# Optimization experiments

Hardware: AMD Instinct MI355X
Metric: run time of the kernel (lower is better)

Reference implementation:

```python
import jax, jax.numpy as jnp
import numpy as np

HEAD = 8
DIM_HEAD = 64
EPS = 1e-5  # torch GroupNorm default


def group_norm(x, w, b, groups, eps=EPS):
    # x: [B, C, H, W]; normalize per (group, spatial)
    B, C, H, W = x.shape
    xg = x.reshape(B, groups, C // groups, H, W)
    mu = xg.mean(axis=(2, 3, 4), keepdims=True)
    var = xg.var(axis=(2, 3, 4), keepdims=True)
    xn = ((xg - mu) / jnp.sqrt(var + eps)).reshape(B, C, H, W)
    return xn * w[None, :, None, None] + b[None, :, None, None]


def setup_inputs() -> dict:
    key = jax.random.key(0)
    ks = jax.random.split(key, 4)
    dim = 256
    hidden = HEAD * DIM_HEAD  # 512
    x = jax.random.normal(ks[0], (16, dim, 64, 64), dtype=jnp.float32)
    qkv_w = jax.random.normal(ks[1], (hidden * 3, dim), dtype=jnp.float32) * 0.02
    out_w = jax.random.normal(ks[2], (dim, hidden), dtype=jnp.float32) * 0.02
    out_b = jnp.zeros((dim,), dtype=jnp.float32)
    gn1_w = jnp.ones((dim,), dtype=jnp.float32)
    gn1_b = jnp.zeros((dim,), dtype=jnp.float32)
    gn2_w = jnp.ones((dim,), dtype=jnp.float32)
    gn2_b = jnp.zeros((dim,), dtype=jnp.float32)
    return {"x": x, "gn1_w": gn1_w, "gn1_b": gn1_b, "qkv_w": qkv_w,
            "out_w": out_w, "out_b": out_b, "gn2_w": gn2_w, "gn2_b": gn2_b}


def reference(x, gn1_w, gn1_b, qkv_w, out_w, out_b, gn2_w, gn2_b):
    B, C, I, J = x.shape
    groups = C // 8
    scale = DIM_HEAD ** -0.5
    n = I * J

    xn = group_norm(x, gn1_w, gn1_b, groups)
    # 1x1 conv == channel matmul: [B,3*hidden,I,J]
    qkv = jnp.einsum('bchw,oc->bohw', xn, qkv_w)
    q, k, v = jnp.split(qkv, 3, axis=1)

    def to_heads(t):  # [B, h*f, I, J] -> [B, h, f, n]
        return t.reshape(B, HEAD, DIM_HEAD, n)

    q = jax.nn.softmax(to_heads(q), axis=-2) * scale  # softmax over feature dim
    k = jax.nn.softmax(to_heads(k), axis=-1)          # softmax over spatial dim
    v = to_heads(v)

    context = jnp.einsum('bhfm,bhem->bhfe', k, v)     # [B,h,f,e]
    attn = jnp.einsum('bhfe,bhfn->bhen', context, q)  # [B,h,e,n]
    out = attn.reshape(B, HEAD * DIM_HEAD, I, J)

    out = jnp.einsum('bchw,oc->bohw', out, out_w) + out_b[None, :, None, None]
    return group_norm(out, gn2_w, gn2_b, groups)
```

## Files before the change

kernel.cpp:

```cpp
#include <hip/hip_runtime.h>
#include <math.h>

#define NB   16
#define NC   256
#define NP   4096
#define NHD  8
#define FD   64
#define HID  512
#define OC3  1536
#define NG   32
#define CPG  8
#define GEPS 1e-5f

typedef __attribute__((ext_vector_type(8))) short bf16x8;
typedef __attribute__((ext_vector_type(4))) float f32x4;

#define MFMA_BF16(a, b, c) __builtin_amdgcn_mfma_f32_16x16x32_bf16(a, b, c, 0, 0, 0)

__device__ __forceinline__ uint bf16_rne(float v) {
    uint u = __float_as_uint(v);
    return (u + 0x7FFFu + ((u >> 16) & 1u)) >> 16;
}
__device__ __forceinline__ void split2(float v, uint& h, uint& l) {
    h = bf16_rne(v);
    l = bf16_rne(v - __uint_as_float(h << 16));
}
__device__ __forceinline__ void gload16(const void* g, void* l) {
    __builtin_amdgcn_global_load_lds(
        (const __attribute__((address_space(1))) void*)g,
        (__attribute__((address_space(3))) void*)l, 16, 0, 0);
}

__global__ __launch_bounds__(256) void gn_stats_kernel(const float* __restrict__ x,
                                                       float* __restrict__ mu,
                                                       float* __restrict__ rstd) {
    int bg = blockIdx.x;
    const float4* b4 = (const float4*)(x + (size_t)bg * CPG * NP);
    int t = threadIdx.x;
    float s = 0.f, sq = 0.f;
    #pragma unroll
    for (int i = 0; i < 32; ++i) {
        float4 v = b4[t + i * 256];
        s  += v.x + v.y + v.z + v.w;
        sq += v.x*v.x + v.y*v.y + v.z*v.z + v.w*v.w;
    }
    for (int off = 32; off; off >>= 1) { s += __shfl_down(s, off); sq += __shfl_down(sq, off); }
    __shared__ float ss[4], ssq[4];
    int wid = t >> 6, lane = t & 63;
    if (lane == 0) { ss[wid] = s; ssq[wid] = sq; }
    __syncthreads();
    if (t == 0) {
        float S  = ss[0] + ss[1] + ss[2] + ss[3];
        float SQ = ssq[0] + ssq[1] + ssq[2] + ssq[3];
        const float inv = 1.f / (float)(CPG * NP);
        float m = S * inv;
        float var = SQ * inv - m * m;
        mu[bg] = m;
        rstd[bg] = rsqrtf(var + GEPS);
    }
}

__global__ void gn1_coefs_kernel(const float* __restrict__ mu, const float* __restrict__ rstd,
                                 const float* __restrict__ w, const float* __restrict__ bias,
                                 float* __restrict__ ac, float* __restrict__ dc) {
    int i = blockIdx.x * 256 + threadIdx.x;
    if (i >= NB * NC) return;
    int b = i / NC, c = i % NC;
    int g = c / CPG;
    float m = mu[b * NG + g], r = rstd[b * NG + g];
    float a = r * w[c];
    ac[i] = a;
    dc[i] = bias[c] - m * a;
}

__global__ void wsplit_kernel(const float* __restrict__ w, ushort* __restrict__ wh,
                              ushort* __restrict__ wl) {
    int i = blockIdx.x * 256 + threadIdx.x;
    float4 v = ((const float4*)w)[i];
    uint h, l;
    ushort4 hv, lv;
    split2(v.x, h, l); hv.x = (ushort)h; lv.x = (ushort)l;
    split2(v.y, h, l); hv.y = (ushort)h; lv.y = (ushort)l;
    split2(v.z, h, l); hv.z = (ushort)h; lv.z = (ushort)l;
    split2(v.w, h, l); hv.w = (ushort)h; lv.w = (ushort)l;
    ((ushort4*)wh)[i] = hv;
    ((ushort4*)wl)[i] = lv;
}

__global__ __launch_bounds__(256) void xsplit_kernel(const float* __restrict__ x,
                                                     const float* __restrict__ ac,
                                                     const float* __restrict__ dc,
                                                     ushort* __restrict__ xTh,
                                                     ushort* __restrict__ xTl, int b0) {
    int z = blockIdx.z, bglob = b0 + z;
    int p0 = blockIdx.x * 64, c0 = blockIdx.y * 64;
    const float* xb = x + (size_t)bglob * NC * NP;
    __shared__ float T[64][68];
    int t = threadIdx.x;
    #pragma unroll
    for (int j = 0; j < 4; ++j) {
        int idx = t + j * 256;
        int r = idx >> 4, c4 = idx & 15;
        float4 v = *(const float4*)(xb + (size_t)(c0 + r) * NP + p0 + c4 * 4);
        float a = ac[bglob * NC + c0 + r], d = dc[bglob * NC + c0 + r];
        v.x = fmaf(v.x, a, d); v.y = fmaf(v.y, a, d);
        v.z = fmaf(v.z, a, d); v.w = fmaf(v.w, a, d);
        *(float4*)&T[r][c4 * 4] = v;
    }
    __syncthreads();
    int p = t & 63, q4 = t >> 6;
    size_t ob = ((size_t)z * NP + p0 + p) * NC + c0 + q4 * 16;
    #pragma unroll
    for (int blk = 0; blk < 2; ++blk) {
        uint4 uh, ul;
        uint* ph = (uint*)&uh; uint* pl = (uint*)&ul;
        #pragma unroll
        for (int i = 0; i < 4; ++i) {
            int c = q4 * 16 + blk * 8 + i * 2;
            uint h0, l0, h1, l1;
            split2(T[c][p], h0, l0);
            split2(T[c + 1][p], h1, l1);
            ph[i] = h0 | (h1 << 16);
            pl[i] = l0 | (l1 << 16);
        }
        *(uint4*)(xTh + ob + blk * 8) = uh;
        *(uint4*)(xTl + ob + blk * 8) = ul;
    }
}

__global__ __launch_bounds__(256) void gemm_q_kernel(
        const ushort* __restrict__ Ah, const ushort* __restrict__ Al,
        const ushort* __restrict__ Bhg, const ushort* __restrict__ Blg,
        ushort* __restrict__ qsTh, ushort* __restrict__ qsTl) {
    __shared__ __align__(16) char smem[33280];
    const int z = blockIdx.z;
    const ushort* Bh = Bhg + (size_t)NP * NC * z;
    const ushort* Bl = Blg + (size_t)NP * NC * z;

    const int t = threadIdx.x;
    const int w = t >> 6, l = t & 63;
    const int wr = w >> 1, wc = w & 1;
    const int m0 = blockIdx.y * 128, n0 = blockIdx.x * 128;
    const int l15 = l & 15, kb = l >> 4;

    f32x4 acc[4][4];
    #pragma unroll
    for (int i = 0; i < 4; ++i)
        #pragma unroll
        for (int j = 0; j < 4; ++j)
            acc[i][j] = (f32x4){0.f, 0.f, 0.f, 0.f};

    for (int k0 = 0; k0 < NC; k0 += 32) {
        #pragma unroll
        for (int j = 0; j < 2; ++j) {
            int idx = t + j * 256;
            int m = idx & 127, s = idx >> 7;
            size_t goA = (size_t)(m0 + m) * NC + k0 + s * 8;
            size_t goB = (size_t)(n0 + m) * NC + k0 + s * 8;
            int lo = idx * 16;
            gload16(Ah + goA, smem + lo);
            gload16(Al + goA, smem + 8192 + lo);
            gload16(Bh + goB, smem + 16384 + lo);
            gload16(Bl + goB, smem + 24576 + lo);
        }
        __syncthreads();
        bf16x8 ah[4], al[4];
        #pragma unroll
        for (int fi = 0; fi < 4; ++fi) {
            int off = (kb * 128 + wr * 64 + fi * 16 + l15) * 16;
            ah[fi] = *(const bf16x8*)(smem + off);
            al[fi] = *(const bf16x8*)(smem + 8192 + off);
        }
        #pragma unroll
        for (int fj = 0; fj < 4; ++fj) {
            int off = (kb * 128 + wc * 64 + fj * 16 + l15) * 16;
            bf16x8 bh = *(const bf16x8*)(smem + 16384 + off);
            bf16x8 bl = *(const bf16x8*)(smem + 24576 + off);
            #pragma unroll
            for (int fi = 0; fi < 4; ++fi) {
                acc[fi][fj] = MFMA_BF16(ah[fi], bh, acc[fi][fj]);
                acc[fi][fj] = MFMA_BF16(al[fi], bh, acc[fi][fj]);
                acc[fi][fj] = MFMA_BF16(ah[fi], bl, acc[fi][fj]);
            }
        }
        __syncthreads();
    }

    uint* Tq = (uint*)smem;
    #pragma unroll
    for (int half = 0; half < 2; ++half) {
        if (wc == half) {
            #pragma unroll
            for (int fj = 0; fj < 4; ++fj) {
                float ex[16];
                float cs = 0.f;
                #pragma unroll
                for (int fi = 0; fi < 4; ++fi)
                    #pragma unroll
                    for (int r = 0; r < 4; ++r) {
                        float e = __expf(acc[fi][fj][r]);
                        ex[fi * 4 + r] = e;
                        cs += e;
                    }
                cs += __shfl_xor(cs, 16);
                cs += __shfl_xor(cs, 32);
                float inv = 0.125f / cs;
                int p_loc = fj * 16 + l15;
                #pragma unroll
                for (int fi = 0; fi < 4; ++fi)
                    #pragma unroll
                    for (int r = 0; r < 4; ++r) {
                        uint hb, lb;
                        split2(ex[fi * 4 + r] * inv, hb, lb);
                        Tq[p_loc * 130 + wr * 64 + fi * 16 + kb * 4 + r] = (hb << 16) | lb;
                    }
            }
        }
        __syncthreads();
        int p = t >> 2, seg = t & 3;
        size_t ob = ((size_t)z * NP + n0 + half * 64 + p) * HID + m0 + seg * 32;
        #pragma unroll
        for (int c = 0; c < 4; ++c) {
            uint4 H, L;
            uint* hp = (uint*)&H; uint* lp = (uint*)&L;
            #pragma unroll
            for (int i = 0; i < 4; ++i) {
                uint u0 = Tq[p * 130 + seg * 32 + c * 8 + 2 * i];
                uint u1 = Tq[p * 130 + seg * 32 + c * 8 + 2 * i + 1];
                hp[i] = (u0 >> 16) | (u1 & 0xffff0000u);
                lp[i] = (u0 & 0xffffu) | (u1 << 16);
            }
            *(uint4*)(qsTh + ob + c * 8) = H;
            *(uint4*)(qsTl + ob + c * 8) = L;
        }
        __syncthreads();
    }
}

__global__ __launch_bounds__(256) void kv_ctx_kernel(
        const ushort* __restrict__ Wh, const ushort* __restrict__ Wl,
        const ushort* __restrict__ Bhg, const ushort* __restrict__ Blg,
        float* __restrict__ ctxp, float* __restrict__ kspart) {
    __shared__ __align__(16) char smem[69632];
    const int z = blockIdx.z;
    const int h = blockIdx.y;
    const int tile = blockIdx.x;
    const int n0 = tile * 128;
    const ushort* Bh = Bhg + (size_t)NP * NC * z;
    const ushort* Bl = Blg + (size_t)NP * NC * z;

    const int t = threadIdx.x;
    const int w = t >> 6, l = t & 63;
    const int wr = w >> 1, wc = w & 1;
    const int l15 = l & 15, kb = l >> 4;

    ushort* ekh = (ushort*)smem;
    ushort* ekl = ekh + 64 * 136;
    ushort* vh_ = ekl + 64 * 136;
    ushort* vl_ = vh_ + 64 * 136;

    f32x4 acc[4][4];
    #pragma unroll
    for (int i = 0; i < 4; ++i)
        #pragma unroll
        for (int j = 0; j < 4; ++j)
            acc[i][j] = (f32x4){0.f, 0.f, 0.f, 0.f};

    for (int k0 = 0; k0 < NC; k0 += 32) {
        #pragma unroll
        for (int j = 0; j < 2; ++j) {
            int idx = t + j * 256;
            int m = idx & 127, s = idx >> 7;
            int grow = 512 + h * 64 + (m & 63) + ((m >> 6) << 9);
            size_t goA = (size_t)grow * NC + k0 + s * 8;
            size_t goB = (size_t)(n0 + m) * NC + k0 + s * 8;
            int lo = idx * 16;
            gload16(Wh + goA, smem + lo);
            gload16(Wl + goA, smem + 8192 + lo);
            gload16(Bh + goB, smem + 16384 + lo);
            gload16(Bl + goB, smem + 24576 + lo);
        }
        __syncthreads();
        bf16x8 ah[4], al[4];
        #pragma unroll
        for (int fi = 0; fi < 4; ++fi) {
            int off = (kb * 128 + wr * 64 + fi * 16 + l15) * 16;
            ah[fi] = *(const bf16x8*)(smem + off);
            al[fi] = *(const bf16x8*)(smem + 8192 + off);
        }
        #pragma unroll
        for (int fj = 0; fj < 4; ++fj) {
            int off = (kb * 128 + wc * 64 + fj * 16 + l15) * 16;
            bf16x8 bh = *(const bf16x8*)(smem + 16384 + off);
            bf16x8 bl = *(const bf16x8*)(smem + 24576 + off);
            #pragma unroll
            for (int fi = 0; fi < 4; ++fi) {
                acc[fi][fj] = MFMA_BF16(ah[fi], bh, acc[fi][fj]);
                acc[fi][fj] = MFMA_BF16(al[fi], bh, acc[fi][fj]);
                acc[fi][fj] = MFMA_BF16(ah[fi], bl, acc[fi][fj]);
            }
        }
        __syncthreads();
    }

    #pragma unroll
    for (int fi = 0; fi < 4; ++fi) {
        #pragma unroll
        for (int r = 0; r < 4; ++r) {
            int row = fi * 16 + kb * 4 + r;
            float rs = 0.f;
            #pragma unroll
            for (int fj = 0; fj < 4; ++fj) {
                float v = acc[fi][fj][r];
                float e = (wr == 0) ? __expf(v) : v;
                rs += e;
                uint hb, lb;
                split2(e, hb, lb);
                int P = wc * 64 + fj * 16 + l15;
                if (wr == 0) { ekh[row * 136 + P] = (ushort)hb; ekl[row * 136 + P] = (ushort)lb; }
                else         { vh_[row * 136 + P] = (ushort)hb; vl_[row * 136 + P] = (ushort)lb; }
            }
            if (wr == 0) {
                rs += __shfl_xor(rs, 1); rs += __shfl_xor(rs, 2);
                rs += __shfl_xor(rs, 4); rs += __shfl_xor(rs, 8);
                if (l15 == 0)
                    kspart[((size_t)z * HID + h * 64 + row) * 64 + tile * 2 + wc] = rs;
            }
        }
    }
    __syncthreads();

    f32x4 c2[2][2];
    #pragma unroll
    for (int i = 0; i < 2; ++i)
        #pragma unroll
        for (int j = 0; j < 2; ++j)
            c2[i][j] = (f32x4){0.f, 0.f, 0.f, 0.f};
    #pragma unroll
    for (int ks = 0; ks < 4; ++ks) {
        bf16x8 a_h[2], a_l[2], b_h[2], b_l[2];
        #pragma unroll
        for (int i = 0; i < 2; ++i) {
            int offa = (wr * 32 + i * 16 + l15) * 136 + ks * 32 + kb * 8;
            a_h[i] = *(const bf16x8*)(ekh + offa);
            a_l[i] = *(const bf16x8*)(ekl + offa);
            int offb = (wc * 32 + i * 16 + l15) * 136 + ks * 32 + kb * 8;
            b_h[i] = *(const bf16x8*)(vh_ + offb);
            b_l[i] = *(const bf16x8*)(vl_ + offb);
        }
        #pragma unroll
        for (int i = 0; i < 2; ++i)
            #pragma unroll
            for (int j = 0; j < 2; ++j) {
                c2[i][j] = MFMA_BF16(a_h[i], b_h[j], c2[i][j]);
                c2[i][j] = MFMA_BF16(a_l[i], b_h[j], c2[i][j]);
                c2[i][j] = MFMA_BF16(a_h[i], b_l[j], c2[i][j]);
            }
    }
    float* outp = ctxp + (((size_t)z * NHD + h) * 32 + tile) * 4096;
    #pragma unroll
    for (int i = 0; i < 2; ++i)
        #pragma unroll
        for (int j = 0; j < 2; ++j)
            #pragma unroll
            for (int r = 0; r < 4; ++r)
                outp[(size_t)(wr * 32 + i * 16 + kb * 4 + r) * 64 + wc * 32 + j * 16 + l15] = c2[i][j][r];
}

__global__ void ksum_reduce_kernel(const float* __restrict__ kspart,
                                   float* __restrict__ ksum, int n) {
    int i = blockIdx.x * 256 + threadIdx.x;
    if (i >= n) return;
    float s = 0.f;
    #pragma unroll
    for (int j = 0; j < 64; ++j) s += kspart[(size_t)i * 64 + j];
    ksum[i] = s;
}

__global__ void ctx_reduce_kernel(const float* __restrict__ ctxp, float* __restrict__ ctx,
                                  int n4) {
    int i = blockIdx.x * 256 + threadIdx.x;
    if (i >= n4) return;
    int zh = i >> 10, i4 = i & 1023;
    const float4* p = (const float4*)ctxp + (size_t)zh * 32 * 1024;
    float4 r = {0.f, 0.f, 0.f, 0.f};
    #pragma unroll
    for (int s = 0; s < 32; ++s) {
        float4 a = p[(size_t)s * 1024 + i4];
        r.x += a.x; r.y += a.y; r.z += a.z; r.w += a.w;
    }
    ((float4*)ctx)[(size_t)zh * 1024 + i4] = r;
}

__global__ __launch_bounds__(256) void fold_kernel(const float* __restrict__ out_w,
                                                   const float* __restrict__ ctx,
                                                   const float* __restrict__ ksum,
                                                   ushort* __restrict__ w2h,
                                                   ushort* __restrict__ w2l) {
    int h = blockIdx.x, z = blockIdx.y;
    __shared__ float Cs[FD][FD];
    int t = threadIdx.x;
    const float* cbase = ctx + ((size_t)z * NHD + h) * FD * FD;
    #pragma unroll
    for (int j = 0; j < 16; ++j) ((float*)Cs)[t + j * 256] = cbase[t + j * 256];
    __syncthreads();
    float wr[64];
    const float* wrow = out_w + (size_t)t * HID + h * FD;
    #pragma unroll
    for (int e = 0; e < 64; ++e) wr[e] = wrow[e];
    size_t ob = ((size_t)z * NC + t) * HID + h * FD;
    for (int f = 0; f < 64; ++f) {
        float sacc = 0.f;
        #pragma unroll
        for (int e = 0; e < 64; ++e) sacc = fmaf(wr[e], Cs[f][e], sacc);
        float v = sacc / ksum[(size_t)z * HID + h * FD + f];
        uint hb, lb;
        split2(v, hb, lb);
        w2h[ob + f] = (ushort)hb;
        w2l[ob + f] = (ushort)lb;
    }
}

__global__ __launch_bounds__(256) void gemm_out_kernel(
        const ushort* __restrict__ Ahg, const ushort* __restrict__ Alg,
        const ushort* __restrict__ Bhg, const ushort* __restrict__ Blg,
        const float* __restrict__ bias, float* __restrict__ outg,
        float2* __restrict__ gn2part, int b0) {
    __shared__ __align__(16) char smem[32768];
    const int z = blockIdx.z, bglob = b0 + z;
    const ushort* Ah = Ahg + (size_t)NC * HID * z;
    const ushort* Al = Alg + (size_t)NC * HID * z;
    const ushort* Bh = Bhg + (size_t)NP * HID * z;
    const ushort* Bl = Blg + (size_t)NP * HID * z;
    float* C = outg + (size_t)bglob * NC * NP;

    const int t = threadIdx.x;
    const int w = t >> 6, l = t & 63;
    const int wr = w >> 1, wc = w & 1;
    const int m0 = blockIdx.y * 128, n0 = blockIdx.x * 128;
    const int l15 = l & 15, kb = l >> 4;

    f32x4 acc[4][4];
    #pragma unroll
    for (int i = 0; i < 4; ++i)
        #pragma unroll
        for (int j = 0; j < 4; ++j)
            acc[i][j] = (f32x4){0.f, 0.f, 0.f, 0.f};

    for (int k0 = 0; k0 < HID; k0 += 32) {
        #pragma unroll
        for (int j = 0; j < 2; ++j) {
            int idx = t + j * 256;
            int m = idx & 127, s = idx >> 7;
            size_t goA = (size_t)(m0 + m) * HID + k0 + s * 8;
            size_t goB = (size_t)(n0 + m) * HID + k0 + s * 8;
            int lo = idx * 16;
            gload16(Ah + goA, smem + lo);
            gload16(Al + goA, smem + 8192 + lo);
            gload16(Bh + goB, smem + 16384 + lo);
            gload16(Bl + goB, smem + 24576 + lo);
        }
        __syncthreads();
        bf16x8 ah[4], al[4];
        #pragma unroll
        for (int fi = 0; fi < 4; ++fi) {
            int off = (kb * 128 + wr * 64 + fi * 16 + l15) * 16;
            ah[fi] = *(const bf16x8*)(smem + off);
            al[fi] = *(const bf16x8*)(smem + 8192 + off);
        }
        #pragma unroll
        for (int fj = 0; fj < 4; ++fj) {
            int off = (kb * 128 + wc * 64 + fj * 16 + l15) * 16;
            bf16x8 bh = *(const bf16x8*)(smem + 16384 + off);
            bf16x8 bl = *(const bf16x8*)(smem + 24576 + off);
            #pragma unroll
            for (int fi = 0; fi < 4; ++fi) {
                acc[fi][fj] = MFMA_BF16(ah[fi], bh, acc[fi][fj]);
                acc[fi][fj] = MFMA_BF16(al[fi], bh, acc[fi][fj]);
                acc[fi][fj] = MFMA_BF16(ah[fi], bl, acc[fi][fj]);
            }
        }
        __syncthreads();
    }

    float gs[4] = {0.f, 0.f, 0.f, 0.f}, gq[4] = {0.f, 0.f, 0.f, 0.f};
    #pragma unroll
    for (int fi = 0; fi < 4; ++fi) {
        int mbase = m0 + wr * 64 + fi * 16 + kb * 4;
        #pragma unroll
        for (int fj = 0; fj < 4; ++fj) {
            int n = n0 + wc * 64 + fj * 16 + l15;
            #pragma unroll
            for (int r = 0; r < 4; ++r) {
                float v = acc[fi][fj][r] + bias[mbase + r];
                C[(size_t)(mbase + r) * NP + n] = v;
                gs[fi] += v;
                gq[fi] += v * v;
            }
        }
    }
    #pragma unroll
    for (int fi = 0; fi < 4; ++fi) {
        #pragma unroll
        for (int d = 1; d <= 16; d <<= 1) {
            gs[fi] += __shfl_xor(gs[fi], d);
            gq[fi] += __shfl_xor(gq[fi], d);
        }
    }
    if (l15 == 0 && (kb & 1) == 0) {
        #pragma unroll
        for (int fi = 0; fi < 4; ++fi) {
            int g = ((m0 + wr * 64) >> 3) + fi * 2 + (kb >> 1);
            float2 pv; pv.x = gs[fi]; pv.y = gq[fi];
            gn2part[(((size_t)bglob * NG + g) << 6) + blockIdx.x * 2 + wc] = pv;
        }
    }
}

__global__ void gn2_reduce_kernel(const float2* __restrict__ gn2part,
                                  float* __restrict__ mu, float* __restrict__ rstd) {
    int i = blockIdx.x * 256 + threadIdx.x;
    if (i >= NB * NG) return;
    float s = 0.f, q = 0.f;
    #pragma unroll
    for (int j = 0; j < 64; ++j) {
        float2 p = gn2part[((size_t)i << 6) + j];
        s += p.x; q += p.y;
    }
    const float inv = 1.f / (float)(CPG * NP);
    float m = s * inv;
    float var = q * inv - m * m;
    mu[i] = m;
    rstd[i] = rsqrtf(var + GEPS);
}

__global__ void gn2_apply_kernel(float* __restrict__ out, const float* __restrict__ mu,
                                 const float* __restrict__ rstd, const float* __restrict__ w,
                                 const float* __restrict__ bias) {
    int i = blockIdx.x * 256 + threadIdx.x;
    float4* p = (float4*)out;
    float4 v = p[i];
    size_t e0 = (size_t)i * 4;
    int cidx = (int)((e0 / NP) % NC);
    int bg   = (int)(e0 / ((size_t)CPG * NP));
    float m = mu[bg], r = rstd[bg];
    float a = r * w[cidx];
    float d = bias[cidx] - m * a;
    v.x = fmaf(v.x, a, d); v.y = fmaf(v.y, a, d);
    v.z = fmaf(v.z, a, d); v.w = fmaf(v.w, a, d);
    p[i] = v;
}

extern "C" void kernel_launch(void* const* d_in, const int* in_sizes, int n_in,
                              void* d_out, int out_size, void* d_ws, size_t ws_size,
                              hipStream_t stream) {
    const float* x     = (const float*)d_in[0];
    const float* gn1_w = (const float*)d_in[1];
    const float* gn1_b = (const float*)d_in[2];
    const float* qkv_w = (const float*)d_in[3];
    const float* out_w = (const float*)d_in[4];
    const float* out_b = (const float*)d_in[5];
    const float* gn2_w = (const float*)d_in[6];
    const float* gn2_b = (const float*)d_in[7];
    float* out = (float*)d_out;

    auto need = [](int cb) -> size_t {
        size_t tot = 0;
        auto al = [&](size_t b) { tot = (tot + b + 255) & ~(size_t)255; };
        al((size_t)cb * NP * NC * 2);  al((size_t)cb * NP * NC * 2);
        al((size_t)cb * NP * HID * 2); al((size_t)cb * NP * HID * 2);
        al((size_t)cb * NHD * 32 * FD * FD * 4);
        al((size_t)cb * NHD * FD * FD * 4);
        al((size_t)cb * HID * 64 * 4);
        al((size_t)cb * HID * 4);
        al((size_t)cb * NC * HID * 2); al((size_t)cb * NC * HID * 2);
        al((size_t)OC3 * NC * 2); al((size_t)OC3 * NC * 2);
        al((size_t)2 * NB * NC * 4);
        al((size_t)4 * NB * NG * 4);
        al((size_t)NB * NG * 64 * 8);
        return tot;
    };
    int CB = 1;
    {
        const int cands[5] = {16, 8, 4, 2, 1};
        for (int i = 0; i < 5; ++i) if (need(cands[i]) <= ws_size) { CB = cands[i]; break; }
    }

    char* base = (char*)d_ws;
    size_t off = 0;
    auto carve = [&](size_t b) -> char* {
        char* p = base + off;
        off = (off + b + 255) & ~(size_t)255;
        return p;
    };
    ushort* xTh  = (ushort*)carve((size_t)CB * NP * NC * 2);
    ushort* xTl  = (ushort*)carve((size_t)CB * NP * NC * 2);
    ushort* qsTh = (ushort*)carve((size_t)CB * NP * HID * 2);
    ushort* qsTl = (ushort*)carve((size_t)CB * NP * HID * 2);
    float*  ctxp = (float*) carve((size_t)CB * NHD * 32 * FD * FD * 4);
    float*  ctx  = (float*) carve((size_t)CB * NHD * FD * FD * 4);
    float*  kspart = (float*)carve((size_t)CB * HID * 64 * 4);
    float*  ksum = (float*) carve((size_t)CB * HID * 4);
    ushort* w2h  = (ushort*)carve((size_t)CB * NC * HID * 2);
    ushort* w2l  = (ushort*)carve((size_t)CB * NC * HID * 2);
    ushort* Wqh  = (ushort*)carve((size_t)OC3 * NC * 2);
    ushort* Wql  = (ushort*)carve((size_t)OC3 * NC * 2);
    float*  ac   = (float*) carve((size_t)2 * NB * NC * 4);
    float*  dc   = ac + (size_t)NB * NC;
    float*  mu1  = (float*) carve((size_t)4 * NB * NG * 4);
    float*  rstd1 = mu1 + NB * NG;
    float*  mu2   = rstd1 + NB * NG;
    float*  rstd2 = mu2 + NB * NG;
    float2* gn2part = (float2*)carve((size_t)NB * NG * 64 * 8);

    gn_stats_kernel<<<NB * NG, 256, 0, stream>>>(x, mu1, rstd1);
    gn1_coefs_kernel<<<16, 256, 0, stream>>>(mu1, rstd1, gn1_w, gn1_b, ac, dc);
    wsplit_kernel<<<OC3 * NC / 1024, 256, 0, stream>>>(qkv_w, Wqh, Wql);

    for (int b0 = 0; b0 < NB; b0 += CB) {
        xsplit_kernel<<<dim3(NP / 64, NC / 64, CB), 256, 0, stream>>>(x, ac, dc, xTh, xTl, b0);
        gemm_q_kernel<<<dim3(NP / 128, 4, CB), 256, 0, stream>>>(Wqh, Wql, xTh, xTl, qsTh, qsTl);
        kv_ctx_kernel<<<dim3(NP / 128, NHD, CB), 256, 0, stream>>>(Wqh, Wql, xTh, xTl, ctxp, kspart);
        ksum_reduce_kernel<<<(CB * HID + 255) / 256, 256, 0, stream>>>(kspart, ksum, CB * HID);
        ctx_reduce_kernel<<<CB * 32, 256, 0, stream>>>(ctxp, ctx, CB * NHD * 1024);
        fold_kernel<<<dim3(NHD, CB), 256, 0, stream>>>(out_w, ctx, ksum, w2h, w2l);
        gemm_out_kernel<<<dim3(NP / 128, 2, CB), 256, 0, stream>>>(
            w2h, w2l, qsTh, qsTl, out_b, out, gn2part, b0);
    }

    gn2_reduce_kernel<<<2, 256, 0, stream>>>(gn2part, mu2, rstd2);
    gn2_apply_kernel<<<16384, 256, 0, stream>>>(out, mu2, rstd2, gn2_w, gn2_b);
}
```

Baseline: 583.6 us.

## Fold GroupNorm1 affine into per-batch QKV weights and fuse stats into split pass

The separate GroupNorm1 stats pass over x is removed. Group statistics are now accumulated inside the transpose/split kernel, which stores raw x as bf16 hi/lo. The per-channel scale is folded into per-batch copies of the QKV weight, and the shift becomes a per-output bias added before the softmax in the q and kv GEMM epilogues. The kv_ctx K-loop also moves to a K-step of 64 with larger shared memory, halving barrier count. This trades one full read of x for per-batch weight splitting and bias kernels, plus more workspace and occupancy pressure in kv_ctx.

Result: slower. 640.8 us (+9.8%).

```diff
diff --git a/kernel.cpp b/kernel.cpp
--- a/kernel.cpp
+++ b/kernel.cpp
@@ -31,109 +31,135 @@
         (__attribute__((address_space(3))) void*)l, 16, 0, 0);
 }
 
-__global__ __launch_bounds__(256) void gn_stats_kernel(const float* __restrict__ x,
-                                                       float* __restrict__ mu,
-                                                       float* __restrict__ rstd) {
-    int bg = blockIdx.x;
-    const float4* b4 = (const float4*)(x + (size_t)bg * CPG * NP);
+__global__ __launch_bounds__(256) void xstats_split_kernel(const float* __restrict__ x,
+                                                           ushort* __restrict__ xTh,
+                                                           ushort* __restrict__ xTl,
+                                                           float2* __restrict__ gn1part, int b0) {
+    int z = blockIdx.z, bglob = b0 + z;
+    int p0 = blockIdx.x * 64, c0 = blockIdx.y * 64;
+    const float* xb = x + (size_t)bglob * NC * NP;
+    __shared__ float T[64][72];
+    __shared__ float rs[64], rq[64];
     int t = threadIdx.x;
-    float s = 0.f, sq = 0.f;
-    #pragma unroll
-    for (int i = 0; i < 32; ++i) {
-        float4 v = b4[t + i * 256];
-        s  += v.x + v.y + v.z + v.w;
-        sq += v.x*v.x + v.y*v.y + v.z*v.z + v.w*v.w;
-    }
-    for (int off = 32; off; off >>= 1) { s += __shfl_down(s, off); sq += __shfl_down(sq, off); }
-    __shared__ float ss[4], ssq[4];
-    int wid = t >> 6, lane = t & 63;
-    if (lane == 0) { ss[wid] = s; ssq[wid] = sq; }
+    #pragma unroll
+    for (int j = 0; j < 4; ++j) {
+        int idx = t + j * 256;
+        int r = idx >> 4, c4 = idx & 15;
+        float4 v = *(const float4*)(xb + (size_t)(c0 + r) * NP + p0 + c4 * 4);
+        *(float4*)&T[r][c4 * 4] = v;
+    }
     __syncthreads();
-    if (t == 0) {
-        float S  = ss[0] + ss[1] + ss[2] + ss[3];
-        float SQ = ssq[0] + ssq[1] + ssq[2] + ssq[3];
-        const float inv = 1.f / (float)(CPG * NP);
-        float m = S * inv;
-        float var = SQ * inv - m * m;
-        mu[bg] = m;
-        rstd[bg] = rsqrtf(var + GEPS);
-    }
+    {
+        int row = t >> 2, quad = t & 3;
+        float s = 0.f, q = 0.f;
+        #pragma unroll
+        for (int j = 0; j < 16; ++j) { float v = T[row][quad * 16 + j]; s += v; q += v * v; }
+        s += __shfl_xor(s, 1); q += __shfl_xor(q, 1);
+        s += __shfl_xor(s, 2); q += __shfl_xor(q, 2);
+        if (quad == 0) { rs[row] = s; rq[row] = q; }
+    }
+    __syncthreads();
+    if (t < 8) {
+        float S = 0.f, Q = 0.f;
+        #pragma unroll
+        for (int k = 0; k < 8; ++k) { S += rs[t * 8 + k]; Q += rq[t * 8 + k]; }
+        gn1part[((size_t)z * NG + blockIdx.y * 8 + t) * 64 + blockIdx.x] = make_float2(S, Q);
+    }
+    int p = t >> 2, cseg = t & 3;
+    size_t ob = ((size_t)z * NP + p0 + p) * NC + c0 + cseg * 16;
+    #pragma unroll
+    for (int half = 0; half < 2; ++half) {
+        uint4 uh, ul;
+        uint* ph = (uint*)&uh; uint* pl = (uint*)&ul;
+        #pragma unroll
+        for (int i = 0; i < 4; ++i) {
+            int c = cseg * 16 + half * 8 + i * 2;
+            uint h0, l0, h1, l1;
+            split2(T[c][p], h0, l0);
+            split2(T[c + 1][p], h1, l1);
+            ph[i] = h0 | (h1 << 16);
+            pl[i] = l0 | (l1 << 16);
+        }
+        *(uint4*)(xTh + ob + half * 8) = uh;
+        *(uint4*)(xTl + ob + half * 8) = ul;
+    }
+}
+
+__global__ void gn1_reduce_kernel(const float2* __restrict__ gn1part,
+                                  float* __restrict__ mu, float* __restrict__ rstd,
+                                  int b0, int n) {
+    int i = blockIdx.x * 256 + threadIdx.x;
+    if (i >= n) return;
+    float S = 0.f, Q = 0.f;
+    #pragma unroll
+    for (int j = 0; j < 64; ++j) {
+        float2 p = gn1part[(size_t)i * 64 + j];
+        S += p.x; Q += p.y;
+    }
+    const float inv = 1.f / (float)(CPG * NP);
+    float m = S * inv;
+    float var = Q * inv - m * m;
+    mu[b0 * NG + i] = m;
+    rstd[b0 * NG + i] = rsqrtf(var + GEPS);
 }
 
 __global__ void gn1_coefs_kernel(const float* __restrict__ mu, const float* __restrict__ rstd,
                                  const float* __restrict__ w, const float* __restrict__ bias,
-                                 float* __restrict__ ac, float* __restrict__ dc) {
+                                 float* __restrict__ ac, float* __restrict__ dc,
+                                 int b0, int n) {
     int i = blockIdx.x * 256 + threadIdx.x;
-    if (i >= NB * NC) return;
-    int b = i / NC, c = i % NC;
+    if (i >= n) return;
+    int bglob = b0 + i / NC, c = i % NC;
     int g = c / CPG;
-    float m = mu[b * NG + g], r = rstd[b * NG + g];
+    float m = mu[bglob * NG + g], r = rstd[bglob * NG + g];
     float a = r * w[c];
-    ac[i] = a;
-    dc[i] = bias[c] - m * a;
-}
-
-__global__ void wsplit_kernel(const float* __restrict__ w, ushort* __restrict__ wh,
-                              ushort* __restrict__ wl) {
-    int i = blockIdx.x * 256 + threadIdx.x;
-    float4 v = ((const float4*)w)[i];
+    ac[(size_t)bglob * NC + c] = a;
+    dc[(size_t)bglob * NC + c] = bias[c] - m * a;
+}
+
+__global__ void wsplit_z_kernel(const float* __restrict__ w, const float* __restrict__ ac,
+                                ushort* __restrict__ Wqzh, ushort* __restrict__ Wqzl, int b0) {
+    int z = blockIdx.y, bglob = b0 + z;
+    int idx = blockIdx.x * 256 + threadIdx.x;
+    float4 v = ((const float4*)w)[idx];
+    int c4 = (idx & 63) * 4;
+    float4 a = *(const float4*)(ac + (size_t)bglob * NC + c4);
+    v.x *= a.x; v.y *= a.y; v.z *= a.z; v.w *= a.w;
     uint h, l;
     ushort4 hv, lv;
     split2(v.x, h, l); hv.x = (ushort)h; lv.x = (ushort)l;
     split2(v.y, h, l); hv.y = (ushort)h; lv.y = (ushort)l;
     split2(v.z, h, l); hv.z = (ushort)h; lv.z = (ushort)l;
     split2(v.w, h, l); hv.w = (ushort)h; lv.w = (ushort)l;
-    ((ushort4*)wh)[i] = hv;
-    ((ushort4*)wl)[i] = lv;
-}
-
-__global__ __launch_bounds__(256) void xsplit_kernel(const float* __restrict__ x,
-                                                     const float* __restrict__ ac,
-                                                     const float* __restrict__ dc,
-                                                     ushort* __restrict__ xTh,
-                                                     ushort* __restrict__ xTl, int b0) {
-    int z = blockIdx.z, bglob = b0 + z;
-    int p0 = blockIdx.x * 64, c0 = blockIdx.y * 64;
-    const float* xb = x + (size_t)bglob * NC * NP;
-    __shared__ float T[64][68];
-    int t = threadIdx.x;
-    #pragma unroll
-    for (int j = 0; j < 4; ++j) {
-        int idx = t + j * 256;
-        int r = idx >> 4, c4 = idx & 15;
-        float4 v = *(const float4*)(xb + (size_t)(c0 + r) * NP + p0 + c4 * 4);
-        float a = ac[bglob * NC + c0 + r], d = dc[bglob * NC + c0 + r];
-        v.x = fmaf(v.x, a, d); v.y = fmaf(v.y, a, d);
-        v.z = fmaf(v.z, a, d); v.w = fmaf(v.w, a, d);
-        *(float4*)&T[r][c4 * 4] = v;
-    }
-    __syncthreads();
-    int p = t & 63, q4 = t >> 6;
-    size_t ob = ((size_t)z * NP + p0 + p) * NC + c0 + q4 * 16;
-    #pragma unroll
-    for (int blk = 0; blk < 2; ++blk) {
-        uint4 uh, ul;
-        uint* ph = (uint*)&uh; uint* pl = (uint*)&ul;
-        #pragma unroll
-        for (int i = 0; i < 4; ++i) {
-            int c = q4 * 16 + blk * 8 + i * 2;
-            uint h0, l0, h1, l1;
-            split2(T[c][p], h0, l0);
-            split2(T[c + 1][p], h1, l1);
-            ph[i] = h0 | (h1 << 16);
-            pl[i] = l0 | (l1 << 16);
-        }
-        *(uint4*)(xTh + ob + blk * 8) = uh;
-        *(uint4*)(xTl + ob + blk * 8) = ul;
-    }
+    ((ushort4*)(Wqzh + (size_t)z * OC3 * NC))[idx] = hv;
+    ((ushort4*)(Wqzl + (size_t)z * OC3 * NC))[idx] = lv;
+}
+
+__global__ void bias2_kernel(const float* __restrict__ w, const float* __restrict__ dc,
+                             float* __restrict__ bias2, int b0) {
+    int i = blockIdx.x * 256 + threadIdx.x;
+    int z = i / OC3, m = i % OC3;
+    int bglob = b0 + z;
+    const float4* w4 = (const float4*)(w + (size_t)m * NC);
+    const float4* d4 = (const float4*)(dc + (size_t)bglob * NC);
+    float s = 0.f;
+    #pragma unroll
+    for (int j = 0; j < 64; ++j) {
+        float4 a = w4[j], b = d4[j];
+        s += a.x * b.x + a.y * b.y + a.z * b.z + a.w * b.w;
+    }
+    bias2[(size_t)z * OC3 + m] = s;
 }
 
 __global__ __launch_bounds__(256) void gemm_q_kernel(
-        const ushort* __restrict__ Ah, const ushort* __restrict__ Al,
+        const ushort* __restrict__ Ahg, const ushort* __restrict__ Alg,
         const ushort* __restrict__ Bhg, const ushort* __restrict__ Blg,
+        const float* __restrict__ bias2,
         ushort* __restrict__ qsTh, ushort* __restrict__ qsTl) {
     __shared__ __align__(16) char smem[33280];
     const int z = blockIdx.z;
+    const ushort* Ah = Ahg + (size_t)OC3 * NC * z;
+    const ushort* Al = Alg + (size_t)OC3 * NC * z;
     const ushort* Bh = Bhg + (size_t)NP * NC * z;
     const ushort* Bl = Blg + (size_t)NP * NC * z;
 
@@ -186,6 +212,16 @@
         __syncthreads();
     }
 
+    float b2v[4][4];
+    {
+        const float* b2z = bias2 + (size_t)z * OC3 + m0 + wr * 64 + kb * 4;
+        #pragma unroll
+        for (int fi = 0; fi < 4; ++fi)
+            #pragma unroll
+            for (int r = 0; r < 4; ++r)
+                b2v[fi][r] = b2z[fi * 16 + r];
+    }
+
     uint* Tq = (uint*)smem;
     #pragma unroll
     for (int half = 0; half < 2; ++half) {
@@ -198,7 +234,7 @@
                 for (int fi = 0; fi < 4; ++fi)
                     #pragma unroll
                     for (int r = 0; r < 4; ++r) {
-                        float e = __expf(acc[fi][fj][r]);
+                        float e = __expf(acc[fi][fj][r] + b2v[fi][r]);
                         ex[fi * 4 + r] = e;
                         cs += e;
                     }
@@ -238,14 +274,17 @@
 }
 
 __global__ __launch_bounds__(256) void kv_ctx_kernel(
-        const ushort* __restrict__ Wh, const ushort* __restrict__ Wl,
+        const ushort* __restrict__ Whg, const ushort* __restrict__ Wlg,
         const ushort* __restrict__ Bhg, const ushort* __restrict__ Blg,
+        const float* __restrict__ bias2,
         float* __restrict__ ctxp, float* __restrict__ kspart) {
     __shared__ __align__(16) char smem[69632];
     const int z = blockIdx.z;
     const int h = blockIdx.y;
     const int tile = blockIdx.x;
     const int n0 = tile * 128;
+    const ushort* Wh = Whg + (size_t)OC3 * NC * z;
+    const ushort* Wl = Wlg + (size_t)OC3 * NC * z;
     const ushort* Bh = Bhg + (size_t)NP * NC * z;
     const ushort* Bl = Blg + (size_t)NP * NC * z;
 
@@ -266,9 +305,9 @@
         for (int j = 0; j < 4; ++j)
             acc[i][j] = (f32x4){0.f, 0.f, 0.f, 0.f};
 
-    for (int k0 = 0; k0 < NC; k0 += 32) {
-        #pragma unroll
-        for (int j = 0; j < 2; ++j) {
+    for (int k0 = 0; k0 < NC; k0 += 64) {
+        #pragma unroll
+        for (int j = 0; j < 4; ++j) {
             int idx = t + j * 256;
             int m = idx & 127, s = idx >> 7;
             int grow = 512 + h * 64 + (m & 63) + ((m >> 6) << 9);
@@ -276,31 +315,44 @@
             size_t goB = (size_t)(n0 + m) * NC + k0 + s * 8;
             int lo = idx * 16;
             gload16(Wh + goA, smem + lo);
-            gload16(Wl + goA, smem + 8192 + lo);
-            gload16(Bh + goB, smem + 16384 + lo);
-            gload16(Bl + goB, smem + 24576 + lo);
-        }
-        __syncthreads();
-        bf16x8 ah[4], al[4];
-        #pragma unroll
-        for (int fi = 0; fi < 4; ++fi) {
-            int off = (kb * 128 + wr * 64 + fi * 16 + l15) * 16;
-            ah[fi] = *(const bf16x8*)(smem + off);
-            al[fi] = *(const bf16x8*)(smem + 8192 + off);
-        }
-        #pragma unroll
-        for (int fj = 0; fj < 4; ++fj) {
-            int off = (kb * 128 + wc * 64 + fj * 16 + l15) * 16;
-            bf16x8 bh = *(const bf16x8*)(smem + 16384 + off);
-            bf16x8 bl = *(const bf16x8*)(smem + 24576 + off);
+            gload16(Wl + goA, smem + 16384 + lo);
+            gload16(Bh + goB, smem + 32768 + lo);
+            gload16(Bl + goB, smem + 49152 + lo);
+        }
+        __syncthreads();
+        #pragma unroll
+        for (int half = 0; half < 2; ++half) {
+            bf16x8 ah[4], al[4];
             #pragma unroll
             for (int fi = 0; fi < 4; ++fi) {
-                acc[fi][fj] = MFMA_BF16(ah[fi], bh, acc[fi][fj]);
-                acc[fi][fj] = MFMA_BF16(al[fi], bh, acc[fi][fj]);
-                acc[fi][fj] = MFMA_BF16(ah[fi], bl, acc[fi][fj]);
-            }
-        }
-        __syncthreads();
+                int off = ((half * 4 + kb) * 128 + wr * 64 + fi * 16 + l15) * 16;
+                ah[fi] = *(const bf16x8*)(smem + off);
+                al[fi] = *(const bf16x8*)(smem + 16384 + off);
+            }
+            #pragma unroll
+            for (int fj = 0; fj < 4; ++fj) {
+                int off = ((half * 4 + kb) * 128 + wc * 64 + fj * 16 + l15) * 16;
+                bf16x8 bh = *(const bf16x8*)(smem + 32768 + off);
+                bf16x8 bl = *(const bf16x8*)(smem + 49152 + off);
+                #pragma unroll
+                for (int fi = 0; fi < 4; ++fi) {
+                    acc[fi][fj] = MFMA_BF16(ah[fi], bh, acc[fi][fj]);
+                    acc[fi][fj] = MFMA_BF16(al[fi], bh, acc[fi][fj]);
+                    acc[fi][fj] = MFMA_BF16(ah[fi], bl, acc[fi][fj]);
+                }
+            }
+        }
+        __syncthreads();
+    }
+
+    float b2v[4][4];
+    {
+        const float* b2z = bias2 + (size_t)z * OC3 + 512 + wr * 512 + h * 64 + kb * 4;
+        #pragma unroll
+        for (int fi = 0; fi < 4; ++fi)
+            #pragma unroll
+            for (int r = 0; r < 4; ++r)
+                b2v[fi][r] = b2z[fi * 16 + r];
     }
 
     #pragma unroll
@@ -311,7 +363,7 @@
             float rs = 0.f;
             #pragma unroll
             for (int fj = 0; fj < 4; ++fj) {
-                float v = acc[fi][fj][r];
+                float v = acc[fi][fj][r] + b2v[fi][r];
                 float e = (wr == 0) ? __expf(v) : v;
                 rs += e;
                 uint hb, lb;
@@ -574,7 +626,9 @@
         al((size_t)cb * HID * 64 * 4);
         al((size_t)cb * HID * 4);
         al((size_t)cb * NC * HID * 2); al((size_t)cb * NC * HID * 2);
-        al((size_t)OC3 * NC * 2); al((size_t)OC3 * NC * 2);
+        al((size_t)cb * OC3 * NC * 2); al((size_t)cb * OC3 * NC * 2);
+        al((size_t)cb * OC3 * 4);
+        al((size_t)cb * NG * 64 * 8);
         al((size_t)2 * NB * NC * 4);
         al((size_t)4 * NB * NG * 4);
         al((size_t)NB * NG * 64 * 8);
@@ -603,8 +657,10 @@
     float*  ksum = (float*) carve((size_t)CB * HID * 4);
     ushort* w2h  = (ushort*)carve((size_t)CB * NC * HID * 2);
     ushort* w2l  = (ushort*)carve((size_t)CB * NC * HID * 2);
-    ushort* Wqh  = (ushort*)carve((size_t)OC3 * NC * 2);
-    ushort* Wql  = (ushort*)carve((size_t)OC3 * NC * 2);
+    ushort* Wqzh = (ushort*)carve((size_t)CB * OC3 * NC * 2);
+    ushort* Wqzl = (ushort*)carve((size_t)CB * OC3 * NC * 2);
+    float*  bias2 = (float*)carve((size_t)CB * OC3 * 4);
+    float2* gn1part = (float2*)carve((size_t)CB * NG * 64 * 8);
     float*  ac   = (float*) carve((size_t)2 * NB * NC * 4);
     float*  dc   = ac + (size_t)NB * NC;
     float*  mu1  = (float*) carve((size_t)4 * NB * NG * 4);
@@ -613,14 +669,19 @@
     float*  rstd2 = mu2 + NB * NG;
     float2* gn2part = (float2*)carve((size_t)NB * NG * 64 * 8);
 
-    gn_stats_kernel<<<NB * NG, 256, 0, stream>>>(x, mu1, rstd1);
-    gn1_coefs_kernel<<<16, 256, 0, stream>>>(mu1, rstd1, gn1_w, gn1_b, ac, dc);
-    wsplit_kernel<<<OC3 * NC / 1024, 256, 0, stream>>>(qkv_w, Wqh, Wql);
-
     for (int b0 = 0; b0 < NB; b0 += CB) {
-        xsplit_kernel<<<dim3(NP / 64, NC / 64, CB), 256, 0, stream>>>(x, ac, dc, xTh, xTl, b0);
-        gemm_q_kernel<<<dim3(NP / 128, 4, CB), 256, 0, stream>>>(Wqh, Wql, xTh, xTl, qsTh, qsTl);
-        kv_ctx_kernel<<<dim3(NP / 128, NHD, CB), 256, 0, stream>>>(Wqh, Wql, xTh, xTl, ctxp, kspart);
+        xstats_split_kernel<<<dim3(NP / 64, NC / 64, CB), 256, 0, stream>>>(
+            x, xTh, xTl, gn1part, b0);
+        gn1_reduce_kernel<<<(CB * NG + 255) / 256, 256, 0, stream>>>(
+            gn1part, mu1, rstd1, b0, CB * NG);
+        gn1_coefs_kernel<<<CB, 256, 0, stream>>>(
+            mu1, rstd1, gn1_w, gn1_b, ac, dc, b0, CB * NC);
+        wsplit_z_kernel<<<dim3(384, CB), 256, 0, stream>>>(qkv_w, ac, Wqzh, Wqzl, b0);
+        bias2_kernel<<<6 * CB, 256, 0, stream>>>(qkv_w, dc, bias2, b0);
+        gemm_q_kernel<<<dim3(NP / 128, 4, CB), 256, 0, stream>>>(
+            Wqzh, Wqzl, xTh, xTl, bias2, qsTh, qsTl);
+        kv_ctx_kernel<<<dim3(NP / 128, NHD, CB), 256, 0, stream>>>(
+            Wqzh, Wqzl, xTh, xTl, bias2, ctxp, kspart);
         ksum_reduce_kernel<<<(CB * HID + 255) / 256, 256, 0, stream>>>(kspart, ksum, CB * HID);
         ctx_reduce_kernel<<<CB * 32, 256, 0, stream>>>(ctxp, ctx, CB * NHD * 1024);
         fold_kernel<<<dim3(NHD, CB), 256, 0, stream>>>(out_w, ctx, ksum, w2h, w2l);
```

## Double kv_ctx block to 512 threads and remap xsplit transpose writes

Applied to the files above, without the earlier changes.

kv_ctx_kernel now runs 8 waves per block instead of 4, each handling a 64x32 slice of the accumulator tile. This halves per-thread accumulator registers and lets more waves hide latency. The k-sum partials grow to 128 per row and the reduction is adjusted to match. xsplit_kernel pads its shared tile to 72 columns and remaps threads so that consecutive threads write adjacent channel segments of the same pixel, which should give more contiguous global stores. The risk is extra block-wide synchronisation and changed shared-memory bank access patterns.

Measured after the change: 564.9 us. -3.2%, faster.

```diff
diff --git a/kernel.cpp b/kernel.cpp
--- a/kernel.cpp
+++ b/kernel.cpp
@@ -95,7 +95,7 @@
     int z = blockIdx.z, bglob = b0 + z;
     int p0 = blockIdx.x * 64, c0 = blockIdx.y * 64;
     const float* xb = x + (size_t)bglob * NC * NP;
-    __shared__ float T[64][68];
+    __shared__ float T[64][72];
     int t = threadIdx.x;
     #pragma unroll
     for (int j = 0; j < 4; ++j) {
@@ -108,23 +108,23 @@
         *(float4*)&T[r][c4 * 4] = v;
     }
     __syncthreads();
-    int p = t & 63, q4 = t >> 6;
-    size_t ob = ((size_t)z * NP + p0 + p) * NC + c0 + q4 * 16;
-    #pragma unroll
-    for (int blk = 0; blk < 2; ++blk) {
+    int p = t >> 2, cseg = t & 3;
+    size_t ob = ((size_t)z * NP + p0 + p) * NC + c0 + cseg * 16;
+    #pragma unroll
+    for (int half = 0; half < 2; ++half) {
         uint4 uh, ul;
         uint* ph = (uint*)&uh; uint* pl = (uint*)&ul;
         #pragma unroll
         for (int i = 0; i < 4; ++i) {
-            int c = q4 * 16 + blk * 8 + i * 2;
+            int c = cseg * 16 + half * 8 + i * 2;
             uint h0, l0, h1, l1;
             split2(T[c][p], h0, l0);
             split2(T[c + 1][p], h1, l1);
             ph[i] = h0 | (h1 << 16);
             pl[i] = l0 | (l1 << 16);
         }
-        *(uint4*)(xTh + ob + blk * 8) = uh;
-        *(uint4*)(xTl + ob + blk * 8) = ul;
+        *(uint4*)(xTh + ob + half * 8) = uh;
+        *(uint4*)(xTl + ob + half * 8) = ul;
     }
 }
 
@@ -237,7 +237,7 @@
     }
 }
 
-__global__ __launch_bounds__(256) void kv_ctx_kernel(
+__global__ __launch_bounds__(512, 4) void kv_ctx_kernel(
         const ushort* __restrict__ Wh, const ushort* __restrict__ Wl,
         const ushort* __restrict__ Bhg, const ushort* __restrict__ Blg,
         float* __restrict__ ctxp, float* __restrict__ kspart) {
@@ -251,7 +251,7 @@
 
     const int t = threadIdx.x;
     const int w = t >> 6, l = t & 63;
-    const int wr = w >> 1, wc = w & 1;
+    const int wr = w >> 2, wc = w & 3;
     const int l15 = l & 15, kb = l >> 4;
 
     ushort* ekh = (ushort*)smem;
@@ -259,17 +259,16 @@
     ushort* vh_ = ekl + 64 * 136;
     ushort* vl_ = vh_ + 64 * 136;
 
-    f32x4 acc[4][4];
+    f32x4 acc[4][2];
     #pragma unroll
     for (int i = 0; i < 4; ++i)
         #pragma unroll
-        for (int j = 0; j < 4; ++j)
+        for (int j = 0; j < 2; ++j)
             acc[i][j] = (f32x4){0.f, 0.f, 0.f, 0.f};
 
     for (int k0 = 0; k0 < NC; k0 += 32) {
-        #pragma unroll
-        for (int j = 0; j < 2; ++j) {
-            int idx = t + j * 256;
+        {
+            int idx = t;
             int m = idx & 127, s = idx >> 7;
             int grow = 512 + h * 64 + (m & 63) + ((m >> 6) << 9);
             size_t goA = (size_t)grow * NC + k0 + s * 8;
@@ -289,8 +288,8 @@
             al[fi] = *(const bf16x8*)(smem + 8192 + off);
         }
         #pragma unroll
-        for (int fj = 0; fj < 4; ++fj) {
-            int off = (kb * 128 + wc * 64 + fj * 16 + l15) * 16;
+        for (int fj = 0; fj < 2; ++fj) {
+            int off = (kb * 128 + wc * 32 + fj * 16 + l15) * 16;
             bf16x8 bh = *(const bf16x8*)(smem + 16384 + off);
             bf16x8 bl = *(const bf16x8*)(smem + 24576 + off);
             #pragma unroll
@@ -310,13 +309,13 @@
             int row = fi * 16 + kb * 4 + r;
             float rs = 0.f;
             #pragma unroll
-            for (int fj = 0; fj < 4; ++fj) {
+            for (int fj = 0; fj < 2; ++fj) {
                 float v = acc[fi][fj][r];
                 float e = (wr == 0) ? __expf(v) : v;
                 rs += e;
                 uint hb, lb;
                 split2(e, hb, lb);
-                int P = wc * 64 + fj * 16 + l15;
+                int P = wc * 32 + fj * 16 + l15;
                 if (wr == 0) { ekh[row * 136 + P] = (ushort)hb; ekl[row * 136 + P] = (ushort)lb; }
                 else         { vh_[row * 136 + P] = (ushort)hb; vl_[row * 136 + P] = (ushort)lb; }
             }
@@ -324,47 +323,42 @@
                 rs += __shfl_xor(rs, 1); rs += __shfl_xor(rs, 2);
                 rs += __shfl_xor(rs, 4); rs += __shfl_xor(rs, 8);
                 if (l15 == 0)
-                    kspart[((size_t)z * HID + h * 64 + row) * 64 + tile * 2 + wc] = rs;
+                    kspart[((size_t)z * HID + h * 64 + row) * 128 + tile * 4 + wc] = rs;
             }
         }
     }
     __syncthreads();
 
-    f32x4 c2[2][2];
-    #pragma unroll
-    for (int i = 0; i < 2; ++i)
-        #pragma unroll
-        for (int j = 0; j < 2; ++j)
-            c2[i][j] = (f32x4){0.f, 0.f, 0.f, 0.f};
+    f32x4 c2[2];
+    c2[0] = (f32x4){0.f, 0.f, 0.f, 0.f};
+    c2[1] = (f32x4){0.f, 0.f, 0.f, 0.f};
+    const int cr0 = (w >> 2) * 32;
+    const int cc0 = (w & 3) * 16;
     #pragma unroll
     for (int ks = 0; ks < 4; ++ks) {
-        bf16x8 a_h[2], a_l[2], b_h[2], b_l[2];
+        bf16x8 a_h[2], a_l[2];
         #pragma unroll
         for (int i = 0; i < 2; ++i) {
-            int offa = (wr * 32 + i * 16 + l15) * 136 + ks * 32 + kb * 8;
+            int offa = (cr0 + i * 16 + l15) * 136 + ks * 32 + kb * 8;
             a_h[i] = *(const bf16x8*)(ekh + offa);
             a_l[i] = *(const bf16x8*)(ekl + offa);
-            int offb = (wc * 32 + i * 16 + l15) * 136 + ks * 32 + kb * 8;
-            b_h[i] = *(const bf16x8*)(vh_ + offb);
-            b_l[i] = *(const bf16x8*)(vl_ + offb);
-        }
-        #pragma unroll
-        for (int i = 0; i < 2; ++i)
-            #pragma unroll
-            for (int j = 0; j < 2; ++j) {
-                c2[i][j] = MFMA_BF16(a_h[i], b_h[j], c2[i][j]);
-                c2[i][j] = MFMA_BF16(a_l[i], b_h[j], c2[i][j]);
-                c2[i][j] = MFMA_BF16(a_h[i], b_l[j], c2[i][j]);
-            }
+        }
+        int offb = (cc0 + l15) * 136 + ks * 32 + kb * 8;
+        bf16x8 b_h = *(const bf16x8*)(vh_ + offb);
+        bf16x8 b_l = *(const bf16x8*)(vl_ + offb);
+        #pragma unroll
+        for (int i = 0; i < 2; ++i) {
+            c2[i] = MFMA_BF16(a_h[i], b_h, c2[i]);
+            c2[i] = MFMA_BF16(a_l[i], b_h, c2[i]);
+            c2[i] = MFMA_BF16(a_h[i], b_l, c2[i]);
+        }
     }
     float* outp = ctxp + (((size_t)z * NHD + h) * 32 + tile) * 4096;
     #pragma unroll
     for (int i = 0; i < 2; ++i)
         #pragma unroll
-        for (int j = 0; j < 2; ++j)
-            #pragma unroll
-            for (int r = 0; r < 4; ++r)
-                outp[(size_t)(wr * 32 + i * 16 + kb * 4 + r) * 64 + wc * 32 + j * 16 + l15] = c2[i][j][r];
+        for (int r = 0; r < 4; ++r)
+            outp[(size_t)(cr0 + i * 16 + kb * 4 + r) * 64 + cc0 + l15] = c2[i][r];
 }
 
 __global__ void ksum_reduce_kernel(const float* __restrict__ kspart,
@@ -373,7 +367,7 @@
     if (i >= n) return;
     float s = 0.f;
     #pragma unroll
-    for (int j = 0; j < 64; ++j) s += kspart[(size_t)i * 64 + j];
+    for (int j = 0; j < 128; ++j) s += kspart[(size_t)i * 128 + j];
     ksum[i] = s;
 }
 
@@ -571,7 +565,7 @@
         al((size_t)cb * NP * HID * 2); al((size_t)cb * NP * HID * 2);
         al((size_t)cb * NHD * 32 * FD * FD * 4);
         al((size_t)cb * NHD * FD * FD * 4);
-        al((size_t)cb * HID * 64 * 4);
+        al((size_t)cb * HID * 128 * 4);
         al((size_t)cb * HID * 4);
         al((size_t)cb * NC * HID * 2); al((size_t)cb * NC * HID * 2);
         al((size_t)OC3 * NC * 2); al((size_t)OC3 * NC * 2);
@@ -599,7 +593,7 @@
     ushort* qsTl = (ushort*)carve((size_t)CB * NP * HID * 2);
     float*  ctxp = (float*) carve((size_t)CB * NHD * 32 * FD * FD * 4);
     float*  ctx  = (float*) carve((size_t)CB * NHD * FD * FD * 4);
-    float*  kspart = (float*)carve((size_t)CB * HID * 64 * 4);
+    float*  kspart = (float*)carve((size_t)CB * HID * 128 * 4);
     float*  ksum = (float*) carve((size_t)CB * HID * 4);
     ushort* w2h  = (ushort*)carve((size_t)CB * NC * HID * 2);
     ushort* w2l  = (ushort*)carve((size_t)CB * NC * HID * 2);
@@ -620,7 +614,7 @@
     for (int b0 = 0; b0 < NB; b0 += CB) {
         xsplit_kernel<<<dim3(NP / 64, NC / 64, CB), 256, 0, stream>>>(x, ac, dc, xTh, xTl, b0);
         gemm_q_kernel<<<dim3(NP / 128, 4, CB), 256, 0, stream>>>(Wqh, Wql, xTh, xTl, qsTh, qsTl);
-        kv_ctx_kernel<<<dim3(NP / 128, NHD, CB), 256, 0, stream>>>(Wqh, Wql, xTh, xTl, ctxp, kspart);
+        kv_ctx_kernel<<<dim3(NP / 128, NHD, CB), 512, 0, stream>>>(Wqh, Wql, xTh, xTl, ctxp, kspart);
         ksum_reduce_kernel<<<(CB * HID + 255) / 256, 256, 0, stream>>>(kspart, ksum, CB * HID);
         ctx_reduce_kernel<<<CB * 32, 256, 0, stream>>>(ctxp, ctx, CB * NHD * 1024);
         fold_kernel<<<dim3(NHD, CB), 256, 0, stream>>>(out_w, ctx, ksum, w2h, w2l);
```
